# Kernel tuning notes

Measured on AMD Instinct MI355X. Metric: run time of the kernel, lower is better.

The kernel has to match this reference:

```python
import jax, jax.numpy as jnp
import numpy as np

EPS = 1e-5

def layer_norm(x, g, b):
    mu = jnp.mean(x, axis=-1, keepdims=True)
    var = jnp.mean((x - mu) ** 2, axis=-1, keepdims=True)
    return (x - mu) * jax.lax.rsqrt(var + EPS) * g + b

def setup_inputs() -> dict:
    key = jax.random.key(0)
    ks = jax.random.split(key, 12)
    P, D_IN, H, D_OUT, N = 2097152, 3, 64, 128, 65536
    x = jax.random.normal(ks[0], (P, D_IN), dtype=jnp.float32)
    batch_idx = jax.random.randint(ks[1], (P,), 0, N, dtype=jnp.int64)
    # mlp1: Linear(3,64) -> LN(64) -> ReLU -> Linear(64,64)
    W1 = jax.random.normal(ks[2], (D_IN, H), dtype=jnp.float32) * (1.0 / np.sqrt(D_IN))
    b1 = jnp.zeros((H,), jnp.float32)
    g1 = jnp.ones((H,), jnp.float32)
    be1 = jnp.zeros((H,), jnp.float32)
    W2 = jax.random.normal(ks[3], (H, H), dtype=jnp.float32) * (1.0 / np.sqrt(H))
    b2 = jnp.zeros((H,), jnp.float32)
    # mlp2: Linear(64,128) -> LN(128) -> ReLU -> Linear(128,128)
    W3 = jax.random.normal(ks[4], (H, D_OUT), dtype=jnp.float32) * (1.0 / np.sqrt(H))
    b3 = jnp.zeros((D_OUT,), jnp.float32)
    g2 = jnp.ones((D_OUT,), jnp.float32)
    be2 = jnp.zeros((D_OUT,), jnp.float32)
    W4 = jax.random.normal(ks[5], (D_OUT, D_OUT), dtype=jnp.float32) * (1.0 / np.sqrt(D_OUT))
    b4 = jnp.zeros((D_OUT,), jnp.float32)
    return {"x": x, "batch_idx": batch_idx, "num_nodes": N,
            "W1": W1, "b1": b1, "g1": g1, "be1": be1, "W2": W2, "b2": b2,
            "W3": W3, "b3": b3, "g2": g2, "be2": be2, "W4": W4, "b4": b4}

def reference(x, batch_idx, num_nodes, W1, b1, g1, be1, W2, b2, W3, b3, g2, be2, W4, b4):
    # per-point MLP1: [P,3] -> [P,64]
    h = jax.nn.relu(layer_norm(x @ W1 + b1, g1, be1)) @ W2 + b2
    # scatter_max pooling over unsorted batch_idx -> [num_nodes, 64]
    seg = jax.ops.segment_max(h, batch_idx, num_segments=num_nodes)
    counts = jax.ops.segment_sum(jnp.ones((h.shape[0],), h.dtype), batch_idx, num_segments=num_nodes)
    # torch_scatter.scatter_max leaves empty segments at 0
    seg = jnp.where(counts[:, None] > 0, seg, 0.0)
    # MLP2: [N,64] -> [N,128]
    out = jax.nn.relu(layer_norm(seg @ W3 + b3, g2, be2)) @ W4 + b4
    return out
```

## Files before the change

### kernel.cpp

```cpp
#include <hip/hip_runtime.h>
#include <hip/hip_bf16.h>
#include <math.h>

#define EPS_LN 1e-5f

typedef __attribute__((ext_vector_type(8))) short bf16x8;
typedef __attribute__((ext_vector_type(4))) float f32x4;
typedef __attribute__((ext_vector_type(2))) unsigned short u16x2;
typedef __attribute__((ext_vector_type(4))) unsigned int u32x4;

__device__ __forceinline__ unsigned short f2bf(float f) {
    __hip_bfloat16 h = __float2bfloat16(f);
    return *reinterpret_cast<unsigned short*>(&h);
}
__device__ __forceinline__ float bf2f(unsigned short u) {
    return __uint_as_float(((unsigned)u) << 16);
}
__device__ __forceinline__ unsigned short ok16(float f) {
    unsigned short t = f2bf(f);
    unsigned short mask = (unsigned short)(((short)t) >> 15);
    return (unsigned short)(t ^ (unsigned short)(mask | 0x8000u));
}
__device__ __forceinline__ float decseg(unsigned o) {
    if (o == 0u) return 0.f;
    unsigned k = o >> 16;
    unsigned h = (k & 0x8000u) ? (k & 0x7FFFu) : (~k & 0xFFFFu);
    return bf2f((unsigned short)h);
}

__global__ __launch_bounds__(256) void prep_kernel(
    const float* __restrict__ W1, const float* __restrict__ b1,
    const float* __restrict__ g1, const float* __restrict__ be1,
    const float* __restrict__ W2,
    const float* __restrict__ W3, const float* __restrict__ W4,
    float* __restrict__ pW1e, float* __restrict__ pGB, float* __restrict__ pSG,
    unsigned short* __restrict__ pW2t,
    unsigned short* __restrict__ W3th, unsigned short* __restrict__ W3tl,
    unsigned short* __restrict__ W4th, unsigned short* __restrict__ W4tl)
{
    const int tid = threadIdx.x;
    if (tid < 64) {
        pW1e[4 * tid + 0] = W1[tid];
        pW1e[4 * tid + 1] = W1[64 + tid];
        pW1e[4 * tid + 2] = W1[128 + tid];
        pW1e[4 * tid + 3] = b1[tid];
        pGB[2 * tid + 0] = g1[tid];
        pGB[2 * tid + 1] = be1[tid];
    }
    if (tid >= 64 && tid < 78) {
        const int t = tid - 64;
        auto wcomp = [&](int k, int i) -> float {
            return (i < 3) ? W1[i * 64 + k] : b1[k];
        };
        if (t < 4) {
            float s = 0.f;
            for (int k = 0; k < 64; k++) s += wcomp(k, t);
            pSG[t] = s;
        } else {
            const int pi[10] = {0,0,0,0,1,1,1,2,2,3};
            const int pj[10] = {0,1,2,3,1,2,3,2,3,3};
            int p = t - 4;
            float s = 0.f;
            for (int k = 0; k < 64; k++) s += wcomp(k, pi[p]) * wcomp(k, pj[p]);
            pSG[4 + p] = s;
        }
    }
    for (int i = tid; i < 4096; i += 256) {
        int k = i >> 6, n = i & 63;
        pW2t[n * 72 + k] = f2bf(W2[i]);
    }
    for (int i = tid; i < 64 * 8; i += 256) {
        int n = i >> 3, k = 64 + (i & 7);
        pW2t[n * 72 + k] = 0;
    }
    for (int i = tid; i < 8192; i += 256) {
        int k = i >> 7, n = i & 127;
        float w = W3[k * 128 + n];
        unsigned short h = f2bf(w);
        W3th[n * 64 + k] = h;
        W3tl[n * 64 + k] = f2bf(w - bf2f(h));
    }
    for (int i = tid; i < 16384; i += 256) {
        int k = i >> 7, n = i & 127;
        float w = W4[k * 128 + n];
        unsigned short h = f2bf(w);
        W4th[n * 128 + k] = h;
        W4tl[n * 128 + k] = f2bf(w - bf2f(h));
    }
}

__global__ __launch_bounds__(256) void s1_count(const int* __restrict__ bidx,
                                                unsigned* __restrict__ blockHist, int P) {
    __shared__ unsigned hist[2048];
    const int tid = threadIdx.x;
    for (int i = tid; i < 2048; i += 256) hist[i] = 0;
    __syncthreads();
    const int base = blockIdx.x * 4096;
#pragma unroll
    for (int j = 0; j < 4; j++) {
        const int p0 = base + j * 1024 + tid * 4;
        if (p0 + 3 < P) {
            int4 n4 = *(const int4*)(bidx + p0);
            atomicAdd(&hist[((unsigned)n4.x) >> 5], 1u);
            atomicAdd(&hist[((unsigned)n4.y) >> 5], 1u);
            atomicAdd(&hist[((unsigned)n4.z) >> 5], 1u);
            atomicAdd(&hist[((unsigned)n4.w) >> 5], 1u);
        } else {
            for (int p = p0; p < P && p < p0 + 4; p++)
                atomicAdd(&hist[((unsigned)bidx[p]) >> 5], 1u);
        }
    }
    __syncthreads();
    unsigned* dst = blockHist + (size_t)blockIdx.x * 2048;
    for (int i = tid; i < 2048; i += 256) dst[i] = hist[i];
}

__global__ __launch_bounds__(256) void s2a_total(const unsigned* __restrict__ blockHist,
                                                 unsigned* __restrict__ binTotal, int nblk) {
    const int bin = blockIdx.x;
    const int tid = threadIdx.x;
    unsigned s = 0;
    for (int b = tid; b < nblk; b += 256) s += blockHist[(size_t)b * 2048 + bin];
    for (int off = 32; off; off >>= 1) s += __shfl_down(s, off);
    __shared__ unsigned ws[4];
    if ((tid & 63) == 0) ws[tid >> 6] = s;
    __syncthreads();
    if (tid == 0) binTotal[bin] = ws[0] + ws[1] + ws[2] + ws[3];
}

__global__ __launch_bounds__(1024) void s2b_scan(const unsigned* __restrict__ binTotal,
                                                 unsigned* __restrict__ partBase,
                                                 int nparts, int P) {
    __shared__ unsigned wtot[16];
    const int t = threadIdx.x;
    const unsigned c0 = (2 * t < nparts) ? binTotal[2 * t] : 0u;
    const unsigned c1 = (2 * t + 1 < nparts) ? binTotal[2 * t + 1] : 0u;
    const unsigned s = c0 + c1;
    unsigned v = s;
    const int lane = t & 63;
    for (int off = 1; off < 64; off <<= 1) {
        unsigned u = __shfl_up(v, off);
        if (lane >= off) v += u;
    }
    if (lane == 63) wtot[t >> 6] = v;
    __syncthreads();
    if (t == 0) {
        unsigned a = 0;
        for (int w = 0; w < 16; w++) { unsigned tmp = wtot[w]; wtot[w] = a; a += tmp; }
    }
    __syncthreads();
    const unsigned excl = wtot[t >> 6] + (v - s);
    if (2 * t < nparts) partBase[2 * t] = excl;
    if (2 * t + 1 < nparts) partBase[2 * t + 1] = excl + c0;
    if (t == 0) partBase[nparts] = (unsigned)P;
}

__global__ __launch_bounds__(256) void s2c_cursor(unsigned* __restrict__ blockHist,
                                                  const unsigned* __restrict__ partBase,
                                                  int nblk) {
    __shared__ unsigned wt0[4], wb0[4], wt1[4], wb1[4], tot0s;
    const int bin = blockIdx.x;
    const int tid = threadIdx.x;
    const int lane = tid & 63;
    const unsigned c0 = (tid < nblk) ? blockHist[(size_t)tid * 2048 + bin] : 0u;
    const unsigned c1 = (tid + 256 < nblk) ? blockHist[(size_t)(tid + 256) * 2048 + bin] : 0u;

    unsigned v0 = c0;
    for (int off = 1; off < 64; off <<= 1) {
        unsigned u = __shfl_up(v0, off);
        if (lane >= off) v0 += u;
    }
    if (lane == 63) wt0[tid >> 6] = v0;
    unsigned v1 = c1;
    for (int off = 1; off < 64; off <<= 1) {
        unsigned u = __shfl_up(v1, off);
        if (lane >= off) v1 += u;
    }
    if (lane == 63) wt1[tid >> 6] = v1;
    __syncthreads();
    if (tid == 0) {
        unsigned a = 0;
        for (int i = 0; i < 4; i++) { unsigned tmp = wt0[i]; wb0[i] = a; a += tmp; }
        tot0s = a;
        a = 0;
        for (int i = 0; i < 4; i++) { unsigned tmp = wt1[i]; wb1[i] = a; a += tmp; }
    }
    __syncthreads();
    const unsigned pb = partBase[bin];
    const unsigned e0 = pb + wb0[tid >> 6] + (v0 - c0);
    const unsigned e1 = pb + tot0s + wb1[tid >> 6] + (v1 - c1);
    if (tid < nblk) blockHist[(size_t)tid * 2048 + bin] = e0;
    if (tid + 256 < nblk) blockHist[(size_t)(tid + 256) * 2048 + bin] = e1;
}

__global__ __launch_bounds__(256) void s3_scatter(const int* __restrict__ bidx,
                                                  const float* __restrict__ x,
                                                  const unsigned* __restrict__ blockCursor,
                                                  float4* __restrict__ xb, int P) {
    __shared__ unsigned cur[2048];
    const int tid = threadIdx.x;
    const unsigned* src = blockCursor + (size_t)blockIdx.x * 2048;
    for (int i = tid; i < 2048; i += 256) cur[i] = src[i];
    __syncthreads();
    const int base = blockIdx.x * 4096;
#pragma unroll
    for (int j = 0; j < 4; j++) {
        const int p0 = base + j * 1024 + tid * 4;
        if (p0 + 3 < P) {
            int4 n4 = *(const int4*)(bidx + p0);
            const float4* xv = (const float4*)(x + 3 * (size_t)p0);
            float4 a = xv[0], b = xv[1], c = xv[2];
            const float xs[12] = {a.x, a.y, a.z, a.w, b.x, b.y, b.z, b.w,
                                  c.x, c.y, c.z, c.w};
            const unsigned nn[4] = {(unsigned)n4.x, (unsigned)n4.y,
                                    (unsigned)n4.z, (unsigned)n4.w};
#pragma unroll
            for (int u = 0; u < 4; u++) {
                const unsigned dst = atomicAdd(&cur[nn[u] >> 5], 1u);
                xb[dst] = make_float4(xs[3 * u], xs[3 * u + 1], xs[3 * u + 2],
                                      __uint_as_float(nn[u]));
            }
        } else {
            for (int u = 0; u < 4; u++) {
                const int p = p0 + u;
                if (p < P) {
                    const unsigned n = (unsigned)bidx[p];
                    const unsigned dst = atomicAdd(&cur[n >> 5], 1u);
                    xb[dst] = make_float4(x[3 * p], x[3 * p + 1], x[3 * p + 2],
                                          __uint_as_float(n));
                }
            }
        }
    }
}

__global__ __launch_bounds__(256) void s4_csr(const unsigned* __restrict__ partBase,
                                              unsigned* __restrict__ offsets,
                                              float4* __restrict__ xb, int N) {
    __shared__ float4 stage[1600];
    __shared__ unsigned hist[32], cur[32];
    const int tid = threadIdx.x;
    const int p = blockIdx.x;
    const unsigned start = partBase[p], end = partBase[p + 1];
    unsigned cnt = end - start;
    if (cnt > 1600u) cnt = 1600u;
    if (tid < 32) hist[tid] = 0;
    __syncthreads();
    for (unsigned k = tid; k < cnt; k += 256) {
        float4 r = xb[start + k];
        stage[k] = r;
        atomicAdd(&hist[__float_as_uint(r.w) & 31u], 1u);
    }
    __syncthreads();
    if (tid < 64) {
        const unsigned c = (tid < 32) ? hist[tid] : 0u;
        unsigned v = c;
        for (int off = 1; off < 32; off <<= 1) {
            unsigned u = __shfl_up(v, off);
            if (tid >= off) v += u;
        }
        if (tid < 32) {
            const unsigned excl = v - c;
            const int node = p * 32 + tid;
            if (node < N) offsets[node] = start + excl;
            cur[tid] = start + excl;
            if (node == N - 1) offsets[N] = start + excl + c;
        }
    }
    __syncthreads();
    for (unsigned k = tid; k < cnt; k += 256) {
        float4 r = stage[k];
        const unsigned dst = atomicAdd(&cur[__float_as_uint(r.w) & 31u], 1u);
        xb[dst] = r;
    }
}

__global__ __launch_bounds__(256, 3) void fused_mlp1_pool_kernel(
    const float4* __restrict__ xb, const unsigned* __restrict__ offsets,
    const float* __restrict__ pW1e, const float* __restrict__ pGB,
    const float* __restrict__ pSG, const unsigned short* __restrict__ pW2t,
    const float* __restrict__ b2,
    unsigned* __restrict__ segord, int P)
{
    __shared__ __align__(16) unsigned short shbt[64 * 260];
    __shared__ unsigned sn01[2];

    const int tid  = threadIdx.x;
    const int wv   = tid >> 6;
    const int lane = tid & 63;
    const int m    = lane & 15;
    const int quad = lane >> 4;
    const int base = blockIdx.x * 256;
    const int pos  = base + tid;
    const bool valid = (pos < P);

    bf16x8 bfrag[4][2];
    float bc[4];
#pragma unroll
    for (int nt = 0; nt < 4; nt++) {
        bc[nt] = b2[nt * 16 + m];
#pragma unroll
        for (int s = 0; s < 2; s++)
            bfrag[nt][s] = *reinterpret_cast<const bf16x8*>(
                &pW2t[(nt * 16 + m) * 72 + s * 32 + quad * 8]);
    }

    float x0 = 0.f, x1 = 0.f, x2 = 0.f;
    if (valid) {
        float4 v = xb[pos];
        x0 = v.x; x1 = v.y; x2 = v.z;
        unsigned node = __float_as_uint(v.w);
        if (tid == 0) sn01[0] = node;
        if (tid == 255 || pos == P - 1) sn01[1] = node;
    }

    float rs, r2;
    {
        const float S0 = pSG[0], S1 = pSG[1], S2 = pSG[2], S3 = pSG[3];
        const float g00 = pSG[4], g01 = pSG[5], g02 = pSG[6], g03 = pSG[7];
        const float g11 = pSG[8], g12 = pSG[9], g13 = pSG[10];
        const float g22 = pSG[11], g23 = pSG[12], g33 = pSG[13];

        const float mu = fmaf(S0, x0, fmaf(S1, x1, fmaf(S2, x2, S3))) * (1.f / 64.f);
        float q = g33;
        q = fmaf(g00, x0 * x0, q);
        q = fmaf(g11, x1 * x1, q);
        q = fmaf(g22, x2 * x2, q);
        float c = fmaf(g01, x1, fmaf(g02, x2, g03));
        q = fmaf(2.f * x0, c, q);
        q = fmaf(2.f * x1, fmaf(g12, x2, g13), q);
        q = fmaf(2.f * x2, g23, q);
        float var = q * (1.f / 64.f) - mu * mu;
        var = var > 0.f ? var : 0.f;
        rs = rsqrtf(var + EPS_LN);
        r2 = -mu * rs;
    }

    float xr0[4], xr1[4], xr2[4], rsr[4], r2r[4];
#pragma unroll
    for (int rt = 0; rt < 4; rt++) {
        const int src = rt * 16 + m;
        xr0[rt] = __shfl(x0, src);
        xr1[rt] = __shfl(x1, src);
        xr2[rt] = __shfl(x2, src);
        rsr[rt] = __shfl(rs, src);
        r2r[rt] = __shfl(r2, src);
    }

    u32x4 afr[4][2];
    {
        const float4* pw = (const float4*)pW1e;
        const float2* pg = (const float2*)pGB;
#pragma unroll
        for (int s = 0; s < 2; s++) {
#pragma unroll
            for (int up = 0; up < 4; up++) {
                const int ch = s * 32 + quad * 8 + up * 2;
                const float4 wA = pw[ch], wB = pw[ch + 1];
                const float2 gA = pg[ch], gB = pg[ch + 1];
#pragma unroll
                for (int rt = 0; rt < 4; rt++) {
                    float y0 = fmaf(xr0[rt], wA.x, fmaf(xr1[rt], wA.y,
                               fmaf(xr2[rt], wA.z, wA.w)));
                    float y1 = fmaf(xr0[rt], wB.x, fmaf(xr1[rt], wB.y,
                               fmaf(xr2[rt], wB.z, wB.w)));
                    float a0 = fmaf(fmaf(y0, rsr[rt], r2r[rt]), gA.x, gA.y);
                    float a1 = fmaf(fmaf(y1, rsr[rt], r2r[rt]), gB.x, gB.y);
                    a0 = a0 > 0.f ? a0 : 0.f;
                    a1 = a1 > 0.f ? a1 : 0.f;
                    afr[rt][s][up] = (unsigned)f2bf(a0) | ((unsigned)f2bf(a1) << 16);
                }
            }
        }
    }

#pragma unroll
    for (int rt = 0; rt < 4; rt++) {
        const int orow = wv * 64 + rt * 16 + quad * 4;
        const bf16x8 af0 = __builtin_bit_cast(bf16x8, afr[rt][0]);
        const bf16x8 af1 = __builtin_bit_cast(bf16x8, afr[rt][1]);
#pragma unroll
        for (int nt = 0; nt < 4; nt++) {
            f32x4 acc = {bc[nt], bc[nt], bc[nt], bc[nt]};
            acc = __builtin_amdgcn_mfma_f32_16x16x32_bf16(af0, bfrag[nt][0], acc, 0, 0, 0);
            acc = __builtin_amdgcn_mfma_f32_16x16x32_bf16(af1, bfrag[nt][1], acc, 0, 0, 0);
            const int col = nt * 16 + m;
            uint2 pk;
            pk.x = (unsigned)ok16(acc[0]) | ((unsigned)ok16(acc[1]) << 16);
            pk.y = (unsigned)ok16(acc[2]) | ((unsigned)ok16(acc[3]) << 16);
            *reinterpret_cast<uint2*>(&shbt[col * 260 + orow]) = pk;
        }
    }
    __syncthreads();

    const int nValid = (P - base < 256) ? (P - base) : 256;
    if (nValid <= 0) return;
    const unsigned n0 = sn01[0];
    const unsigned n1 = sn01[1];
    const unsigned bEnd = (unsigned)(base + nValid);
    const int wave = tid >> 6;
    const int ch   = tid & 63;
    const unsigned short* rowp = &shbt[ch * 260];

    for (unsigned n = n0 + (unsigned)wave; n <= n1; n += 4) {
        const unsigned s = offsets[n];
        const unsigned e = offsets[n + 1];
        int lo = (int)(s > (unsigned)base ? s : (unsigned)base) - base;
        int hi = (int)(e < bEnd ? e : bEnd) - base;
        if (hi <= lo) continue;
        u16x2 accv = {0, 0};
        unsigned short accs = 0;
        for (int r = lo & ~3; r < hi; r += 4) {
            uint2 d = *reinterpret_cast<const uint2*>(rowp + r);
            if (r >= lo && r + 4 <= hi) {
                u16x2 a = __builtin_bit_cast(u16x2, d.x);
                u16x2 b = __builtin_bit_cast(u16x2, d.y);
                accv = __builtin_elementwise_max(accv, __builtin_elementwise_max(a, b));
            } else {
                unsigned short v0 = (unsigned short)(d.x & 0xFFFFu);
                unsigned short v1 = (unsigned short)(d.x >> 16);
                unsigned short v2 = (unsigned short)(d.y & 0xFFFFu);
                unsigned short v3 = (unsigned short)(d.y >> 16);
                if (r     >= lo && r     < hi && v0 > accs) accs = v0;
                if (r + 1 >= lo && r + 1 < hi && v1 > accs) accs = v1;
                if (r + 2 >= lo && r + 2 < hi && v2 > accs) accs = v2;
                if (r + 3 >= lo && r + 3 < hi && v3 > accs) accs = v3;
            }
        }
        unsigned short k = accv.x > accv.y ? accv.x : accv.y;
        if (accs > k) k = accs;
        const unsigned key = ((unsigned)k) << 16;
        unsigned* dst = &segord[(size_t)n * 64 + ch];
        if (s >= (unsigned)base && e <= bEnd) *dst = key;
        else atomicMax(dst, key);
    }
}

__global__ __launch_bounds__(256) void mlp2_mfma_kernel(
    const unsigned* __restrict__ segord,
    const unsigned short* __restrict__ W3th, const unsigned short* __restrict__ W3tl,
    const unsigned short* __restrict__ W4th, const unsigned short* __restrict__ W4tl,
    const float* __restrict__ b3, const float* __restrict__ g2,
    const float* __restrict__ be2, const float* __restrict__ b4,
    float* __restrict__ out, int N)
{
    __shared__ __align__(16) unsigned short sa2[32 * 72];
    __shared__ __align__(16) float st[32 * 132];
    __shared__ __align__(16) unsigned short suh[32 * 136];
    __shared__ __align__(16) unsigned short sul[32 * 136];
    __shared__ float2 sred[32][8];
    __shared__ float sg2[128], sbe2[128];

    const int tid  = threadIdx.x;
    const int wv   = tid >> 6;
    const int lane = tid & 63;
    const int m    = lane & 15;
    const int quad = lane >> 4;

    if (tid < 128) { sg2[tid] = g2[tid]; sbe2[tid] = be2[tid]; }

    bf16x8 fw3h[2][2], fw3l[2][2];
    bf16x8 fw4h[2][4], fw4l[2][4];
    float bias3[2], bias4[2];
#pragma unroll
    for (int nti = 0; nti < 2; nti++) {
        const int nrow = (wv * 2 + nti) * 16 + m;
        bias3[nti] = b3[nrow];
        bias4[nti] = b4[nrow];
#pragma unroll
        for (int ks = 0; ks < 2; ks++) {
            fw3h[nti][ks] = *reinterpret_cast<const bf16x8*>(&W3th[nrow * 64 + ks * 32 + quad * 8]);
            fw3l[nti][ks] = *reinterpret_cast<const bf16x8*>(&W3tl[nrow * 64 + ks * 32 + quad * 8]);
        }
#pragma unroll
        for (int ks = 0; ks < 4; ks++) {
            fw4h[nti][ks] = *reinterpret_cast<const bf16x8*>(&W4th[nrow * 128 + ks * 32 + quad * 8]);
            fw4l[nti][ks] = *reinterpret_cast<const bf16x8*>(&W4tl[nrow * 128 + ks * 32 + quad * 8]);
        }
    }
    __syncthreads();

    for (int nb = blockIdx.x * 32; nb < N; nb += gridDim.x * 32) {
        {
            const int node = tid >> 3;
            const int k8   = (tid & 7) * 8;
            const uint4* sp = (const uint4*)&segord[(size_t)(nb + node) * 64 + k8];
            uint4 q0 = sp[0], q1 = sp[1];
            bf16x8 v;
            v[0] = (short)f2bf(decseg(q0.x));
            v[1] = (short)f2bf(decseg(q0.y));
            v[2] = (short)f2bf(decseg(q0.z));
            v[3] = (short)f2bf(decseg(q0.w));
            v[4] = (short)f2bf(decseg(q1.x));
            v[5] = (short)f2bf(decseg(q1.y));
            v[6] = (short)f2bf(decseg(q1.z));
            v[7] = (short)f2bf(decseg(q1.w));
            *reinterpret_cast<bf16x8*>(&sa2[node * 72 + k8]) = v;
        }
        __syncthreads();

#pragma unroll
        for (int mt = 0; mt < 2; mt++) {
            bf16x8 a0 = *reinterpret_cast<const bf16x8*>(&sa2[(mt * 16 + m) * 72 + quad * 8]);
            bf16x8 a1 = *reinterpret_cast<const bf16x8*>(&sa2[(mt * 16 + m) * 72 + 32 + quad * 8]);
#pragma unroll
            for (int nti = 0; nti < 2; nti++) {
                f32x4 acc = {bias3[nti], bias3[nti], bias3[nti], bias3[nti]};
                acc = __builtin_amdgcn_mfma_f32_16x16x32_bf16(a0, fw3h[nti][0], acc, 0, 0, 0);
                acc = __builtin_amdgcn_mfma_f32_16x16x32_bf16(a1, fw3h[nti][1], acc, 0, 0, 0);
                acc = __builtin_amdgcn_mfma_f32_16x16x32_bf16(a0, fw3l[nti][0], acc, 0, 0, 0);
                acc = __builtin_amdgcn_mfma_f32_16x16x32_bf16(a1, fw3l[nti][1], acc, 0, 0, 0);
#pragma unroll
                for (int r = 0; r < 4; r++)
                    st[(mt * 16 + quad * 4 + r) * 132 + (wv * 2 + nti) * 16 + m] = acc[r];
            }
        }
        __syncthreads();

        {
            const int node = tid >> 3;
            const int seg  = tid & 7;
            const float4* rp = (const float4*)&st[node * 132 + seg * 16];
            float4 v0 = rp[0], v1 = rp[1], v2 = rp[2], v3 = rp[3];
            float s1 = v0.x + v0.y + v0.z + v0.w + v1.x + v1.y + v1.z + v1.w
                     + v2.x + v2.y + v2.z + v2.w + v3.x + v3.y + v3.z + v3.w;
            float s2 = 0.f;
            s2 = fmaf(v0.x, v0.x, s2); s2 = fmaf(v0.y, v0.y, s2); s2 = fmaf(v0.z, v0.z, s2); s2 = fmaf(v0.w, v0.w, s2);
            s2 = fmaf(v1.x, v1.x, s2); s2 = fmaf(v1.y, v1.y, s2); s2 = fmaf(v1.z, v1.z, s2); s2 = fmaf(v1.w, v1.w, s2);
            s2 = fmaf(v2.x, v2.x, s2); s2 = fmaf(v2.y, v2.y, s2); s2 = fmaf(v2.z, v2.z, s2); s2 = fmaf(v2.w, v2.w, s2);
            s2 = fmaf(v3.x, v3.x, s2); s2 = fmaf(v3.y, v3.y, s2); s2 = fmaf(v3.z, v3.z, s2); s2 = fmaf(v3.w, v3.w, s2);
            sred[node][seg] = make_float2(s1, s2);
            __syncthreads();

            float t1 = 0.f, t2 = 0.f;
#pragma unroll
            for (int i = 0; i < 8; i++) { float2 r = sred[node][i]; t1 += r.x; t2 += r.y; }
            const float mu  = t1 * (1.f / 128.f);
            float var = t2 * (1.f / 128.f) - mu * mu;
            var = var > 0.f ? var : 0.f;
            const float rsd = rsqrtf(var + EPS_LN);

            float tv[16] = {v0.x, v0.y, v0.z, v0.w, v1.x, v1.y, v1.z, v1.w,
                            v2.x, v2.y, v2.z, v2.w, v3.x, v3.y, v3.z, v3.w};
            bf16x8 vh[2], vl[2];
#pragma unroll
            for (int i = 0; i < 16; i++) {
                const int j = seg * 16 + i;
                float u = fmaf((tv[i] - mu) * rsd, sg2[j], sbe2[j]);
                u = u > 0.f ? u : 0.f;
                unsigned short uh = f2bf(u);
                unsigned short ul = f2bf(u - bf2f(uh));
                vh[i >> 3][i & 7] = (short)uh;
                vl[i >> 3][i & 7] = (short)ul;
            }
            *reinterpret_cast<bf16x8*>(&suh[node * 136 + seg * 16])     = vh[0];
            *reinterpret_cast<bf16x8*>(&suh[node * 136 + seg * 16 + 8]) = vh[1];
            *reinterpret_cast<bf16x8*>(&sul[node * 136 + seg * 16])     = vl[0];
            *reinterpret_cast<bf16x8*>(&sul[node * 136 + seg * 16 + 8]) = vl[1];
        }
        __syncthreads();

#pragma unroll
        for (int mt = 0; mt < 2; mt++) {
            bf16x8 ah[4], al[4];
#pragma unroll
            for (int ks = 0; ks < 4; ks++) {
                ah[ks] = *reinterpret_cast<const bf16x8*>(&suh[(mt * 16 + m) * 136 + ks * 32 + quad * 8]);
                al[ks] = *reinterpret_cast<const bf16x8*>(&sul[(mt * 16 + m) * 136 + ks * 32 + quad * 8]);
            }
#pragma unroll
            for (int nti = 0; nti < 2; nti++) {
                f32x4 acc = {bias4[nti], bias4[nti], bias4[nti], bias4[nti]};
#pragma unroll
                for (int ks = 0; ks < 4; ks++) {
                    acc = __builtin_amdgcn_mfma_f32_16x16x32_bf16(ah[ks], fw4h[nti][ks], acc, 0, 0, 0);
                    acc = __builtin_amdgcn_mfma_f32_16x16x32_bf16(al[ks], fw4h[nti][ks], acc, 0, 0, 0);
                    acc = __builtin_amdgcn_mfma_f32_16x16x32_bf16(ah[ks], fw4l[nti][ks], acc, 0, 0, 0);
                }
#pragma unroll
                for (int r = 0; r < 4; r++) {
                    const int node = nb + mt * 16 + quad * 4 + r;
                    if (node < N)
                        out[(size_t)node * 128 + (wv * 2 + nti) * 16 + m] = acc[r];
                }
            }
        }
        __syncthreads();
    }
}

extern "C" void kernel_launch(void* const* d_in, const int* in_sizes, int n_in,
                              void* d_out, int out_size, void* d_ws, size_t ws_size,
                              hipStream_t stream) {
    const float* x    = (const float*)d_in[0];
    const int*   bidx = (const int*)d_in[1];
    const float* W1  = (const float*)d_in[3];
    const float* b1  = (const float*)d_in[4];
    const float* g1  = (const float*)d_in[5];
    const float* be1 = (const float*)d_in[6];
    const float* W2  = (const float*)d_in[7];
    const float* b2  = (const float*)d_in[8];
    const float* W3  = (const float*)d_in[9];
    const float* b3  = (const float*)d_in[10];
    const float* g2  = (const float*)d_in[11];
    const float* be2 = (const float*)d_in[12];
    const float* W4  = (const float*)d_in[13];
    const float* b4  = (const float*)d_in[14];

    const int P = in_sizes[0] / 3;
    const int N = out_size / 128;
    const int nparts = (N + 31) >> 5;
    const int nblk   = (P + 4095) / 4096;

    uintptr_t w = (uintptr_t)d_ws;
    auto align = [](uintptr_t v) { return (v + 255) & ~(uintptr_t)255; };
    unsigned* blockHist = (unsigned*)align(w);     w = (uintptr_t)(blockHist + (size_t)nblk * 2048);
    unsigned* binTotal  = (unsigned*)align(w);     w = (uintptr_t)(binTotal  + 2048);
    unsigned* partBase  = (unsigned*)align(w);     w = (uintptr_t)(partBase  + 2049);
    unsigned* offsets   = (unsigned*)align(w);     w = (uintptr_t)(offsets   + N + 1);
    float4*   xb        = (float4*)align(w);       w = (uintptr_t)(xb        + P);
    unsigned* segord    = (unsigned*)align(w);     w = (uintptr_t)(segord    + (size_t)N * 64);
    float*    pW1e      = (float*)align(w);        w = (uintptr_t)(pW1e      + 256);
    float*    pGB       = (float*)align(w);        w = (uintptr_t)(pGB       + 128);
    float*    pSG       = (float*)align(w);        w = (uintptr_t)(pSG       + 16);
    unsigned short* pW2t = (unsigned short*)align(w); w = (uintptr_t)(pW2t + 64 * 72);
    unsigned short* W3th = (unsigned short*)align(w); w = (uintptr_t)(W3th + 128 * 64);
    unsigned short* W3tl = (unsigned short*)align(w); w = (uintptr_t)(W3tl + 128 * 64);
    unsigned short* W4th = (unsigned short*)align(w); w = (uintptr_t)(W4th + 128 * 128);
    unsigned short* W4tl = (unsigned short*)align(w); w = (uintptr_t)(W4tl + 128 * 128);

    hipMemsetAsync(segord, 0, (size_t)N * 64 * sizeof(unsigned), stream);

    prep_kernel<<<1, 256, 0, stream>>>(W1, b1, g1, be1, W2, W3, W4,
                                       pW1e, pGB, pSG, pW2t, W3th, W3tl, W4th, W4tl);

    s1_count<<<nblk, 256, 0, stream>>>(bidx, blockHist, P);
    s2a_total<<<nparts, 256, 0, stream>>>(blockHist, binTotal, nblk);
    s2b_scan<<<1, 1024, 0, stream>>>(binTotal, partBase, nparts, P);
    s2c_cursor<<<nparts, 256, 0, stream>>>(blockHist, partBase, nblk);
    s3_scatter<<<nblk, 256, 0, stream>>>(bidx, x, blockHist, xb, P);
    s4_csr<<<nparts, 256, 0, stream>>>(partBase, offsets, xb, N);

    fused_mlp1_pool_kernel<<<(P + 255) / 256, 256, 0, stream>>>(
        xb, offsets, pW1e, pGB, pSG, pW2t, b2, segord, P);

    mlp2_mfma_kernel<<<2048, 256, 0, stream>>>(
        segord, W3th, W3tl, W4th, W4tl, b3, g2, be2, b4, (float*)d_out, N);
}
```

Baseline: 350.1 us.

## Replace two-level bucketed counting sort with global-atomic per-node CSR build

Replaces the block-histogram, multi-kernel radix partition and the per-partition CSR refinement with a direct per-node count using global atomics, a single-block scan over all nodes, and a scatter using global atomic cursors. This cuts the kernel count and drops the large blockHist buffer plus the second local reorder pass. In exchange it issues millions of global atomics on random addresses in both count and scatter, and the scan runs serially within a single block. It also reduces the mlp2 grid from 2048 to 512 blocks.

```diff
diff --git a/kernel.cpp b/kernel.cpp
--- a/kernel.cpp
+++ b/kernel.cpp
@@ -89,119 +89,65 @@
     }
 }
 
-__global__ __launch_bounds__(256) void s1_count(const int* __restrict__ bidx,
-                                                unsigned* __restrict__ blockHist, int P) {
-    __shared__ unsigned hist[2048];
-    const int tid = threadIdx.x;
-    for (int i = tid; i < 2048; i += 256) hist[i] = 0;
-    __syncthreads();
-    const int base = blockIdx.x * 4096;
-#pragma unroll
-    for (int j = 0; j < 4; j++) {
-        const int p0 = base + j * 1024 + tid * 4;
-        if (p0 + 3 < P) {
-            int4 n4 = *(const int4*)(bidx + p0);
-            atomicAdd(&hist[((unsigned)n4.x) >> 5], 1u);
-            atomicAdd(&hist[((unsigned)n4.y) >> 5], 1u);
-            atomicAdd(&hist[((unsigned)n4.z) >> 5], 1u);
-            atomicAdd(&hist[((unsigned)n4.w) >> 5], 1u);
-        } else {
-            for (int p = p0; p < P && p < p0 + 4; p++)
-                atomicAdd(&hist[((unsigned)bidx[p]) >> 5], 1u);
-        }
-    }
-    __syncthreads();
-    unsigned* dst = blockHist + (size_t)blockIdx.x * 2048;
-    for (int i = tid; i < 2048; i += 256) dst[i] = hist[i];
-}
-
-__global__ __launch_bounds__(256) void s2a_total(const unsigned* __restrict__ blockHist,
-                                                 unsigned* __restrict__ binTotal, int nblk) {
-    const int bin = blockIdx.x;
-    const int tid = threadIdx.x;
+__global__ __launch_bounds__(256) void c1_count(const int* __restrict__ bidx,
+                                                unsigned* __restrict__ nodeCount, int P) {
+    const int p0 = blockIdx.x * 1024 + threadIdx.x * 4;
+    if (p0 + 3 < P) {
+        int4 n4 = *(const int4*)(bidx + p0);
+        atomicAdd(&nodeCount[(unsigned)n4.x], 1u);
+        atomicAdd(&nodeCount[(unsigned)n4.y], 1u);
+        atomicAdd(&nodeCount[(unsigned)n4.z], 1u);
+        atomicAdd(&nodeCount[(unsigned)n4.w], 1u);
+    } else {
+        for (int p = p0; p < P && p < p0 + 4; p++)
+            atomicAdd(&nodeCount[(unsigned)bidx[p]], 1u);
+    }
+}
+
+__global__ __launch_bounds__(1024) void c2_scan(const unsigned* __restrict__ nodeCount,
+                                                unsigned* __restrict__ offsets,
+                                                unsigned* __restrict__ cursor,
+                                                int N, int P) {
+    __shared__ unsigned wsum[16];
+    const int t = threadIdx.x;
+    const int CH = (N + 1023) >> 10;
+    const int b0 = t * CH;
+
     unsigned s = 0;
-    for (int b = tid; b < nblk; b += 256) s += blockHist[(size_t)b * 2048 + bin];
-    for (int off = 32; off; off >>= 1) s += __shfl_down(s, off);
-    __shared__ unsigned ws[4];
-    if ((tid & 63) == 0) ws[tid >> 6] = s;
-    __syncthreads();
-    if (tid == 0) binTotal[bin] = ws[0] + ws[1] + ws[2] + ws[3];
-}
-
-__global__ __launch_bounds__(1024) void s2b_scan(const unsigned* __restrict__ binTotal,
-                                                 unsigned* __restrict__ partBase,
-                                                 int nparts, int P) {
-    __shared__ unsigned wtot[16];
-    const int t = threadIdx.x;
-    const unsigned c0 = (2 * t < nparts) ? binTotal[2 * t] : 0u;
-    const unsigned c1 = (2 * t + 1 < nparts) ? binTotal[2 * t + 1] : 0u;
-    const unsigned s = c0 + c1;
+    for (int i = 0; i < CH; i++) {
+        const int idx = b0 + i;
+        if (idx < N) s += nodeCount[idx];
+    }
     unsigned v = s;
     const int lane = t & 63;
     for (int off = 1; off < 64; off <<= 1) {
         unsigned u = __shfl_up(v, off);
         if (lane >= off) v += u;
     }
-    if (lane == 63) wtot[t >> 6] = v;
+    if (lane == 63) wsum[t >> 6] = v;
     __syncthreads();
     if (t == 0) {
         unsigned a = 0;
-        for (int w = 0; w < 16; w++) { unsigned tmp = wtot[w]; wtot[w] = a; a += tmp; }
+        for (int w = 0; w < 16; w++) { unsigned tmp = wsum[w]; wsum[w] = a; a += tmp; }
     }
     __syncthreads();
-    const unsigned excl = wtot[t >> 6] + (v - s);
-    if (2 * t < nparts) partBase[2 * t] = excl;
-    if (2 * t + 1 < nparts) partBase[2 * t + 1] = excl + c0;
-    if (t == 0) partBase[nparts] = (unsigned)P;
-}
-
-__global__ __launch_bounds__(256) void s2c_cursor(unsigned* __restrict__ blockHist,
-                                                  const unsigned* __restrict__ partBase,
-                                                  int nblk) {
-    __shared__ unsigned wt0[4], wb0[4], wt1[4], wb1[4], tot0s;
-    const int bin = blockIdx.x;
+    unsigned run = wsum[t >> 6] + (v - s);
+    for (int i = 0; i < CH; i++) {
+        const int idx = b0 + i;
+        if (idx < N) {
+            offsets[idx] = run;
+            cursor[idx]  = run;
+            run += nodeCount[idx];
+        }
+    }
+    if (t == 0) offsets[N] = (unsigned)P;
+}
+
+__global__ __launch_bounds__(256) void c3_scatter(const int* __restrict__ bidx,
+                                                  const float* __restrict__ x,
+                                                  unsigned* __restrict__ cursor,
+                                                  float4* __restrict__ xb, int P) {
     const int tid = threadIdx.x;
-    const int lane = tid & 63;
-    const unsigned c0 = (tid < nblk) ? blockHist[(size_t)tid * 2048 + bin] : 0u;
-    const unsigned c1 = (tid + 256 < nblk) ? blockHist[(size_t)(tid + 256) * 2048 + bin] : 0u;
-
-    unsigned v0 = c0;
-    for (int off = 1; off < 64; off <<= 1) {
-        unsigned u = __shfl_up(v0, off);
-        if (lane >= off) v0 += u;
-    }
-    if (lane == 63) wt0[tid >> 6] = v0;
-    unsigned v1 = c1;
-    for (int off = 1; off < 64; off <<= 1) {
-        unsigned u = __shfl_up(v1, off);
-        if (lane >= off) v1 += u;
-    }
-    if (lane == 63) wt1[tid >> 6] = v1;
-    __syncthreads();
-    if (tid == 0) {
-        unsigned a = 0;
-        for (int i = 0; i < 4; i++) { unsigned tmp = wt0[i]; wb0[i] = a; a += tmp; }
-        tot0s = a;
-        a = 0;
-        for (int i = 0; i < 4; i++) { unsigned tmp = wt1[i]; wb1[i] = a; a += tmp; }
-    }
-    __syncthreads();
-    const unsigned pb = partBase[bin];
-    const unsigned e0 = pb + wb0[tid >> 6] + (v0 - c0);
-    const unsigned e1 = pb + tot0s + wb1[tid >> 6] + (v1 - c1);
-    if (tid < nblk) blockHist[(size_t)tid * 2048 + bin] = e0;
-    if (tid + 256 < nblk) blockHist[(size_t)(tid + 256) * 2048 + bin] = e1;
-}
-
-__global__ __launch_bounds__(256) void s3_scatter(const int* __restrict__ bidx,
-                                                  const float* __restrict__ x,
-                                                  const unsigned* __restrict__ blockCursor,
-                                                  float4* __restrict__ xb, int P) {
-    __shared__ unsigned cur[2048];
-    const int tid = threadIdx.x;
-    const unsigned* src = blockCursor + (size_t)blockIdx.x * 2048;
-    for (int i = tid; i < 2048; i += 256) cur[i] = src[i];
-    __syncthreads();
     const int base = blockIdx.x * 4096;
 #pragma unroll
     for (int j = 0; j < 4; j++) {
@@ -216,7 +162,7 @@
                                     (unsigned)n4.z, (unsigned)n4.w};
 #pragma unroll
             for (int u = 0; u < 4; u++) {
-                const unsigned dst = atomicAdd(&cur[nn[u] >> 5], 1u);
+                const unsigned dst = atomicAdd(&cursor[nn[u]], 1u);
                 xb[dst] = make_float4(xs[3 * u], xs[3 * u + 1], xs[3 * u + 2],
                                       __uint_as_float(nn[u]));
             }
@@ -225,53 +171,12 @@
                 const int p = p0 + u;
                 if (p < P) {
                     const unsigned n = (unsigned)bidx[p];
-                    const unsigned dst = atomicAdd(&cur[n >> 5], 1u);
+                    const unsigned dst = atomicAdd(&cursor[n], 1u);
                     xb[dst] = make_float4(x[3 * p], x[3 * p + 1], x[3 * p + 2],
                                           __uint_as_float(n));
                 }
             }
         }
-    }
-}
-
-__global__ __launch_bounds__(256) void s4_csr(const unsigned* __restrict__ partBase,
-                                              unsigned* __restrict__ offsets,
-                                              float4* __restrict__ xb, int N) {
-    __shared__ float4 stage[1600];
-    __shared__ unsigned hist[32], cur[32];
-    const int tid = threadIdx.x;
-    const int p = blockIdx.x;
-    const unsigned start = partBase[p], end = partBase[p + 1];
-    unsigned cnt = end - start;
-    if (cnt > 1600u) cnt = 1600u;
-    if (tid < 32) hist[tid] = 0;
-    __syncthreads();
-    for (unsigned k = tid; k < cnt; k += 256) {
-        float4 r = xb[start + k];
-        stage[k] = r;
-        atomicAdd(&hist[__float_as_uint(r.w) & 31u], 1u);
-    }
-    __syncthreads();
-    if (tid < 64) {
-        const unsigned c = (tid < 32) ? hist[tid] : 0u;
-        unsigned v = c;
-        for (int off = 1; off < 32; off <<= 1) {
-            unsigned u = __shfl_up(v, off);
-            if (tid >= off) v += u;
-        }
-        if (tid < 32) {
-            const unsigned excl = v - c;
-            const int node = p * 32 + tid;
-            if (node < N) offsets[node] = start + excl;
-            cur[tid] = start + excl;
-            if (node == N - 1) offsets[N] = start + excl + c;
-        }
-    }
-    __syncthreads();
-    for (unsigned k = tid; k < cnt; k += 256) {
-        float4 r = stage[k];
-        const unsigned dst = atomicAdd(&cur[__float_as_uint(r.w) & 31u], 1u);
-        xb[dst] = r;
     }
 }
 
@@ -609,14 +514,13 @@
 
     const int P = in_sizes[0] / 3;
     const int N = out_size / 128;
-    const int nparts = (N + 31) >> 5;
-    const int nblk   = (P + 4095) / 4096;
+    const int nblkC = (P + 1023) / 1024;
+    const int nblkS = (P + 4095) / 4096;
 
     uintptr_t w = (uintptr_t)d_ws;
     auto align = [](uintptr_t v) { return (v + 255) & ~(uintptr_t)255; };
-    unsigned* blockHist = (unsigned*)align(w);     w = (uintptr_t)(blockHist + (size_t)nblk * 2048);
-    unsigned* binTotal  = (unsigned*)align(w);     w = (uintptr_t)(binTotal  + 2048);
-    unsigned* partBase  = (unsigned*)align(w);     w = (uintptr_t)(partBase  + 2049);
+    unsigned* nodeCount = (unsigned*)align(w);     w = (uintptr_t)(nodeCount + N);
+    unsigned* cursor    = (unsigned*)align(w);     w = (uintptr_t)(cursor    + N);
     unsigned* offsets   = (unsigned*)align(w);     w = (uintptr_t)(offsets   + N + 1);
     float4*   xb        = (float4*)align(w);       w = (uintptr_t)(xb        + P);
     unsigned* segord    = (unsigned*)align(w);     w = (uintptr_t)(segord    + (size_t)N * 64);
@@ -629,21 +533,19 @@
     unsigned short* W4th = (unsigned short*)align(w); w = (uintptr_t)(W4th + 128 * 128);
     unsigned short* W4tl = (unsigned short*)align(w); w = (uintptr_t)(W4tl + 128 * 128);
 
+    hipMemsetAsync(nodeCount, 0, (size_t)N * sizeof(unsigned), stream);
     hipMemsetAsync(segord, 0, (size_t)N * 64 * sizeof(unsigned), stream);
 
     prep_kernel<<<1, 256, 0, stream>>>(W1, b1, g1, be1, W2, W3, W4,
                                        pW1e, pGB, pSG, pW2t, W3th, W3tl, W4th, W4tl);
 
-    s1_count<<<nblk, 256, 0, stream>>>(bidx, blockHist, P);
-    s2a_total<<<nparts, 256, 0, stream>>>(blockHist, binTotal, nblk);
-    s2b_scan<<<1, 1024, 0, stream>>>(binTotal, partBase, nparts, P);
-    s2c_cursor<<<nparts, 256, 0, stream>>>(blockHist, partBase, nblk);
-    s3_scatter<<<nblk, 256, 0, stream>>>(bidx, x, blockHist, xb, P);
-    s4_csr<<<nparts, 256, 0, stream>>>(partBase, offsets, xb, N);
+    c1_count<<<nblkC, 256, 0, stream>>>(bidx, nodeCount, P);
+    c2_scan<<<1, 1024, 0, stream>>>(nodeCount, offsets, cursor, N, P);
+    c3_scatter<<<nblkS, 256, 0, stream>>>(bidx, x, cursor, xb, P);
 
     fused_mlp1_pool_kernel<<<(P + 255) / 256, 256, 0, stream>>>(
         xb, offsets, pW1e, pGB, pSG, pW2t, b2, segord, P);
 
-    mlp2_mfma_kernel<<<2048, 256, 0, stream>>>(
+    mlp2_mfma_kernel<<<512, 256, 0, stream>>>(
         segord, W3th, W3tl, W4th, W4tl, b3, g2, be2, b4, (float*)d_out, N);
 }
```

New measurement: 630.0 us. 1.8x slower.
